# Kernel optimization log

Measured on AMD Instinct MI355X. Metric: run time of the kernel, lower is better.

## Reference

```python
import jax, jax.numpy as jnp
import numpy as np

B_GRAPHS = 256      # graphs per batch
NPG = 256           # nodes per graph
EXTENT = 32.0       # coordinate extent
K1 = 5              # kernel size per dim
KK = K1 * K1        # 25 weight matrices (dim=2)


def _cartesian(pos, row, col, ev):
    # pseudo-coords: relative cartesian, globally rescaled into [0,1]
    d = pos[col] - pos[row]                                   # [E,2]
    m = jnp.max(jnp.where(ev[:, None] > 0, jnp.abs(d), 0.0))
    return d / (2.0 * m + 1e-12) + 0.5


def _spline_conv(x, row, col, pseudo, ev, W, root, bias, n):
    # degree-1 open B-spline basis, 4 nonzero corners per edge (dim=2)
    v = pseudo * (K1 - 1)
    i0 = jnp.clip(jnp.floor(v), 0, K1 - 2).astype(jnp.int32)  # [E,2]
    f = v - i0
    xin = x[col]                                              # [E,Fin] gather
    acc = jnp.zeros((n * KK, x.shape[1]), x.dtype)
    for sx in (0, 1):
        for sy in (0, 1):
            idx = (i0[:, 0] + sx) * K1 + (i0[:, 1] + sy)      # flat kernel id
            wx = f[:, 0] if sx else 1.0 - f[:, 0]
            wy = f[:, 1] if sy else 1.0 - f[:, 1]
            b = wx * wy * ev
            acc = acc.at[row * KK + idx].add(b[:, None] * xin)
    acc = acc.reshape(n, KK, x.shape[1])                      # [n,25,Fin]
    deg = jax.ops.segment_sum(ev, row, num_segments=n)
    out = jnp.einsum('nki,kio->no', acc, W) / jnp.maximum(deg, 1.0)[:, None]
    return out + x @ root + bias


def _grid_pool(x, pos, row, col, ev, nv, size):
    g = int(EXTENT // size)
    c = jnp.clip(jnp.floor(pos / size).astype(jnp.int32), 0, g - 1)
    cluster = (jnp.arange(x.shape[0], dtype=jnp.int32) * 0)  # placeholder
    cell = c[:, 0] * g + c[:, 1]
    nb = x.shape[0] // 1  # nodes
    # batch id of each node = node's graph; recover from fixed layout
    # (cluster id = graph * g*g + cell)
    per_graph = nb // B_GRAPHS
    gb = jnp.arange(nb, dtype=jnp.int32) // per_graph
    cluster = gb * (g * g) + cell
    Nc = B_GRAPHS * g * g
    seg = jnp.where(nv > 0, cluster, Nc)                      # invalid -> dummy
    xm = jax.ops.segment_max(jnp.where(nv[:, None] > 0, x, -jnp.inf), seg,
                             num_segments=Nc + 1)[:Nc]
    cnt = jax.ops.segment_sum(nv, seg, num_segments=Nc + 1)[:Nc]
    nv2 = (cnt > 0).astype(x.dtype)
    x2 = jnp.where(nv2[:, None] > 0, xm, 0.0)
    pos2 = jax.ops.segment_sum(pos * nv[:, None], seg, num_segments=Nc + 1)[:Nc]
    pos2 = pos2 / jnp.maximum(cnt, 1.0)[:, None]
    batch2 = jnp.arange(Nc, dtype=jnp.int32) // (g * g)
    # remap + coalesce edges (drop self-loops and duplicates, fixed shapes)
    r2 = cluster[row]
    c2 = cluster[col]
    ev2 = (ev > 0) & (r2 != c2)
    key = jnp.where(ev2, r2 * Nc + c2, Nc * Nc)
    order = jnp.argsort(key)
    skey = key[order]
    dup = jnp.concatenate([jnp.zeros((1,), bool), skey[1:] == skey[:-1]])
    ev3 = ((skey < Nc * Nc) & ~dup).astype(x.dtype)
    return x2, pos2, r2[order], c2[order], ev3, batch2, nv2


def _forward(x, position, edge_index, batch, W1, root1, b1, W2, root2, b2,
             W3, root3, b3, fc_w, fc_b):
    row, col = edge_index[0], edge_index[1]
    E, N = row.shape[0], x.shape[0]
    ev = jnp.ones((E,), x.dtype)
    nv = jnp.ones((N,), x.dtype)
    ps = _cartesian(position, row, col, ev)
    h = jax.nn.elu(_spline_conv(x, row, col, ps, ev, W1, root1, b1, N))
    h, pos, row, col, ev, batch2, nv = _grid_pool(h, position, row, col, ev, nv, 4.0)
    ps = _cartesian(pos, row, col, ev)
    h = jax.nn.elu(_spline_conv(h, row, col, ps, ev, W2, root2, b2, h.shape[0]))
    h, pos, row, col, ev, batch2, nv = _grid_pool(h, pos, row, col, ev, nv, 8.0)
    ps = _cartesian(pos, row, col, ev)
    h = jax.nn.elu(_spline_conv(h, row, col, ps, ev, W3, root3, b3, h.shape[0]))
    # scatter_mean over graphs (only non-empty clusters count)
    gsum = jax.ops.segment_sum(h * nv[:, None], batch2, num_segments=B_GRAPHS)
    gcnt = jax.ops.segment_sum(nv, batch2, num_segments=B_GRAPHS)
    gfeat = gsum / jnp.maximum(gcnt, 1.0)[:, None]
    # dropout is identity in eval mode
    logits = gfeat @ fc_w + fc_b
    return jax.nn.log_softmax(logits, axis=1)


def setup_inputs() -> dict:
    DEG = 16
    N = B_GRAPHS * NPG
    E = N * DEG
    key = jax.random.key(0)
    ks = jax.random.split(key, 14)
    x = jax.random.uniform(ks[0], (N, 1), jnp.float32)
    position = jax.random.uniform(ks[1], (N, 2), jnp.float32) * EXTENT
    src = jax.random.randint(ks[2], (E,), 0, N, dtype=jnp.int32)
    tgt = (src // NPG) * NPG + jax.random.randint(ks[3], (E,), 0, NPG, dtype=jnp.int32)
    edge_index = jnp.stack([tgt, src])  # row = target, col = source
    batch = jnp.arange(N, dtype=jnp.int32) // NPG
    s = 0.1
    W1 = jax.random.normal(ks[4], (KK, 1, 32), jnp.float32) * s
    root1 = jax.random.normal(ks[5], (1, 32), jnp.float32) * s
    b1 = jnp.zeros((32,), jnp.float32)
    W2 = jax.random.normal(ks[6], (KK, 32, 64), jnp.float32) * s
    root2 = jax.random.normal(ks[7], (32, 64), jnp.float32) * s
    b2 = jnp.zeros((64,), jnp.float32)
    W3 = jax.random.normal(ks[8], (KK, 64, 128), jnp.float32) * s
    root3 = jax.random.normal(ks[9], (64, 128), jnp.float32) * s
    b3 = jnp.zeros((128,), jnp.float32)
    fc_w = jax.random.normal(ks[10], (128, 10), jnp.float32) * s
    fc_b = jnp.zeros((10,), jnp.float32)
    return dict(x=x, position=position, edge_index=edge_index, batch=batch,
                W1=W1, root1=root1, b1=b1, W2=W2, root2=root2, b2=b2,
                W3=W3, root3=root3, b3=b3, fc_w=fc_w, fc_b=fc_b)


def reference(x, position, edge_index, batch, W1, root1, b1, W2, root2, b2,
              W3, root3, b3, fc_w, fc_b):
    return _forward(x, position, edge_index, batch, W1, root1, b1,
                    W2, root2, b2, W3, root3, b3, fc_w, fc_b)
```

## Files before the change

### kernel.cpp

```cpp
#include <hip/hip_runtime.h>
#include <math.h>

constexpr int NN  = 65536;
constexpr int EE  = 1048576;
constexpr int NG  = 256;
constexpr int NC1 = 16384;
constexpr int NC2 = 4096;
constexpr int EPB = EE / 256;

constexpr size_t O_SCAL  = 0;
constexpr size_t O_GTOT  = 256;
constexpr size_t O_CNT2  = O_GTOT + 1024;
constexpr size_t O_PS2   = O_CNT2 + (size_t)NC2*4;
constexpr size_t Z_END   = O_PS2  + (size_t)NC2*8;
constexpr size_t O_XM2   = Z_END;
constexpr size_t O_GOFF  = O_XM2  + (size_t)NC2*64*4;
constexpr size_t O_BB    = O_GOFF + 1280;
constexpr size_t O_BE    = O_BB   + (size_t)256*256*4;
constexpr size_t O_XP1   = O_BE   + (size_t)EE*2;
constexpr size_t O_POS1  = O_XP1  + (size_t)NC1*32*4;
constexpr size_t O_NV1   = O_POS1 + (size_t)NC1*8;
constexpr size_t O_ADJ2  = O_NV1  + (size_t)NC1*4;
constexpr size_t O_OFF2S = O_ADJ2 + (size_t)NG*4096;
constexpr size_t O_DEG2I = O_OFF2S+ (size_t)NC1*4;
constexpr size_t O_CL2   = O_DEG2I+ (size_t)NC1*4;
constexpr size_t O_XP2   = O_CL2  + (size_t)NC1*4;
constexpr size_t O_POS2  = O_XP2  + (size_t)NC2*64*4;
constexpr size_t O_NV2   = O_POS2 + (size_t)NC2*8;
constexpr size_t O_ADJ3  = O_NV2  + (size_t)NC2*4;
constexpr size_t O_OFF3S = O_ADJ3 + (size_t)NG*256;
constexpr size_t O_DEG3I = O_OFF3S+ (size_t)NC2*4;
constexpr size_t O_H3    = O_DEG3I+ (size_t)NC2*4;
constexpr size_t O_W2Q   = O_H3   + (size_t)NC2*128*4;
constexpr size_t O_W3Q   = O_W2Q  + 102400;
constexpr size_t O_R2T   = O_W3Q  + 409600;
constexpr size_t O_R3T   = O_R2T  + 8192;

typedef __fp16   pk16x2 __attribute__((ext_vector_type(2)));
typedef _Float16 h16x2  __attribute__((ext_vector_type(2)));

__device__ __forceinline__ float eluf(float x){ return x > 0.f ? x : expm1f(x); }

__device__ __forceinline__ void atomic_max_pos(float* a, float v){
    atomicMax((unsigned int*)a, __float_as_uint(v));
}
__device__ __forceinline__ void atomic_max_f32(float* a, float v){
    unsigned int b = __float_as_uint(v);
    if (b & 0x80000000u) atomicMin((unsigned int*)a, b);
    else                 atomicMax((int*)a, (int)b);
}

__device__ __forceinline__ unsigned int pack2(float a, float b){
    pk16x2 h = __builtin_amdgcn_cvt_pkrtz(a, b);
    return __builtin_bit_cast(unsigned int, h);
}
__device__ __forceinline__ unsigned short f2h(float v){
    pk16x2 h = __builtin_amdgcn_cvt_pkrtz(v, v);
    return (unsigned short)(__builtin_bit_cast(unsigned int, h) & 0xFFFFu);
}
__device__ __forceinline__ float dot2u(unsigned int a, unsigned int b, float c){
#if __has_builtin(__builtin_amdgcn_fdot2)
    return __builtin_amdgcn_fdot2(__builtin_bit_cast(h16x2, a),
                                  __builtin_bit_cast(h16x2, b), c, false);
#else
    h16x2 ha = __builtin_bit_cast(h16x2, a), hb = __builtin_bit_cast(h16x2, b);
    return c + (float)ha[0]*(float)hb[0] + (float)ha[1]*(float)hb[1];
#endif
}

struct Crn { int ix, iy; float fx, fy; };
__device__ __forceinline__ Crn mk_corners(float dx, float dy, float m){
    float inv = 1.0f / (2.0f*m + 1e-12f);
    float vx = (dx*inv + 0.5f) * 4.0f;
    float vy = (dy*inv + 0.5f) * 4.0f;
    Crn c;
    c.ix = min(max((int)floorf(vx), 0), 3);
    c.iy = min(max((int)floorf(vy), 0), 3);
    c.fx = vx - (float)c.ix;
    c.fy = vy - (float)c.iy;
    return c;
}

#define BLOCK_MAX_AND_ATOMIC(val, dst)                                   \
    {   __shared__ float _s[256];                                        \
        _s[threadIdx.x] = (val); __syncthreads();                        \
        for (int _w = 128; _w > 0; _w >>= 1){                            \
            if (threadIdx.x < _w)                                        \
                _s[threadIdx.x] = fmaxf(_s[threadIdx.x], _s[threadIdx.x+_w]); \
            __syncthreads();                                             \
        }                                                                \
        if (threadIdx.x == 0) atomic_max_pos((dst), _s[0]); }

__global__ __launch_bounds__(256) void k_pass1(
        const int* __restrict__ ei, const float* __restrict__ pos,
        float* m1, int* gtot, int* bb,
        const float* __restrict__ W2, const float* __restrict__ W3,
        const float* __restrict__ root2, const float* __restrict__ root3,
        unsigned short* __restrict__ w2q, unsigned short* __restrict__ w3q,
        float* __restrict__ r2t, float* __restrict__ r3t){
    __shared__ int h[256];
    if (blockIdx.x >= 256){
        int idx = (blockIdx.x - 256)*256 + threadIdx.x;
        if (idx < 51200){
            int k = idx >> 6, o = idx & 63;
            w2q[(size_t)((k>>3)*64 + o)*8 + (k&7)] = f2h(W2[idx]);
        }
        int i3 = idx - 51200;
        if (i3 >= 0 && i3 < 204800){
            int k = i3 >> 7, o = i3 & 127;
            w3q[(size_t)((k>>3)*128 + o)*8 + (k&7)] = f2h(W3[i3]);
        }
        int ir2 = idx - 256000;
        if (ir2 >= 0 && ir2 < 2048){
            int i = ir2 >> 6, o = ir2 & 63;
            r2t[o*32 + i] = root2[ir2];
        }
        int ir3 = idx - 258048;
        if (ir3 >= 0 && ir3 < 8192){
            int i = ir3 >> 7, o = ir3 & 127;
            r3t[o*64 + i] = root3[ir3];
        }
        return;
    }
    h[threadIdx.x] = 0; __syncthreads();
    int base = blockIdx.x * EPB;
    float loc = 0.f;
    for (int i = threadIdx.x; i < EPB; i += 256){
        int e = base + i;
        int r = ei[e], c = ei[EE + e];
        float dx = pos[2*c]   - pos[2*r];
        float dy = pos[2*c+1] - pos[2*r+1];
        loc = fmaxf(loc, fmaxf(fabsf(dx), fabsf(dy)));
        atomicAdd(&h[r >> 8], 1);
    }
    __syncthreads();
    bb[blockIdx.x*256 + threadIdx.x] = atomicAdd(&gtot[threadIdx.x], h[threadIdx.x]);
    BLOCK_MAX_AND_ATOMIC(loc, m1);
}

__global__ void k_gscan(const int* __restrict__ gtot, int* goff){
    __shared__ int s[256];
    int t = threadIdx.x;
    int v0 = gtot[t];
    s[t] = v0; __syncthreads();
    for (int d = 1; d < 256; d <<= 1){
        int u = (t >= d) ? s[t-d] : 0;
        __syncthreads();
        s[t] += u;
        __syncthreads();
    }
    goff[t] = s[t] - v0;
    if (t == 255) goff[256] = s[t];
}

__global__ __launch_bounds__(256) void k_pass2(const int* __restrict__ ei,
                                               const int* __restrict__ goff,
                                               const int* __restrict__ bb,
                                               unsigned short* __restrict__ be){
    __shared__ int cur[256];
    cur[threadIdx.x] = 0; __syncthreads();
    int base = blockIdx.x * EPB;
    for (int i = threadIdx.x; i < EPB; i += 256){
        int e = base + i;
        int r = ei[e], c = ei[EE + e];
        int g = r >> 8;
        int l = atomicAdd(&cur[g], 1);
        be[goff[g] + bb[blockIdx.x*256 + g] + l] =
            (unsigned short)((r & 255) | ((c & 255) << 8));
    }
}

__global__ __launch_bounds__(1024) void k_graph1(
        const unsigned short* __restrict__ be, const int* __restrict__ goff,
        const float* __restrict__ pos, const float* __restrict__ x,
        const float* __restrict__ m1p, const float* __restrict__ W1,
        const float* __restrict__ root1, const float* __restrict__ b1,
        float* __restrict__ xp1, float* __restrict__ pos1g, float* __restrict__ nv1,
        unsigned char* __restrict__ adj2b, int* __restrict__ off2s,
        int* __restrict__ deg2i, float* m2p){
    __shared__ float acc[256*25];
    __shared__ float posx[256], posy[256], xL[256];
    __shared__ int   cl1L[256], degL[256];
    __shared__ float sW[800];
    __shared__ unsigned int bitL[128];
    __shared__ float xmL[64*32];
    __shared__ int   cntL[64];
    __shared__ float psx[64], psy[64];
    __shared__ float p1x[64], p1y[64];
    __shared__ int   rpre[64];
    __shared__ float mred[64];

    int t = threadIdx.x, g = blockIdx.x;
    if (t < 800) sW[t] = W1[t];
    for (int i = t; i < 6400; i += 1024) acc[i] = 0.f;
    if (t < 256){
        float px = pos[2*(g*256 + t)], py = pos[2*(g*256 + t) + 1];
        posx[t] = px; posy[t] = py;
        xL[t]   = x[g*256 + t];
        degL[t] = 0;
        int cx = min(max((int)floorf(px*0.25f), 0), 7);
        int cy = min(max((int)floorf(py*0.25f), 0), 7);
        cl1L[t] = cx*8 + cy;
    }
    if (t < 128) bitL[t] = 0u;
    if (t < 64){ cntL[t] = 0; psx[t] = 0.f; psy[t] = 0.f; }
    for (int i = t; i < 2048; i += 1024) xmL[i] = -INFINITY;
    __syncthreads();

    float mm = *m1p;
    int e1 = goff[g+1];
    for (int p = goff[g] + t; p < e1; p += 1024){
        unsigned int b = be[p];
        int rl = b & 255, cl = (b >> 8) & 255;
        float dx = posx[cl] - posx[rl], dy = posy[cl] - posy[rl];
        Crn cr = mk_corners(dx, dy, mm);
        float xin = xL[cl];
        int ab = rl*25 + cr.ix*5 + cr.iy;
        atomicAdd(&acc[ab],   (1.f-cr.fx)*(1.f-cr.fy)*xin);
        atomicAdd(&acc[ab+1], (1.f-cr.fx)*cr.fy*xin);
        atomicAdd(&acc[ab+5], cr.fx*(1.f-cr.fy)*xin);
        atomicAdd(&acc[ab+6], cr.fx*cr.fy*xin);
        atomicAdd(&degL[rl], 1);
        int r2 = cl1L[rl], c2 = cl1L[cl];
        if (r2 != c2){
            int bit = r2*64 + c2;
            atomicOr(&bitL[bit >> 5], 1u << (bit & 31));
        }
    }
    __syncthreads();

    {
        int n = t >> 2, q = t & 3;
        float accR[25];
        #pragma unroll
        for (int k = 0; k < 25; k++) accR[k] = acc[n*25 + k];
        float inv = 1.f / fmaxf((float)degL[n], 1.f);
        float xr  = xL[n];
        int   cl  = cl1L[n];
        if (q == 0){
            atomicAdd(&cntL[cl], 1);
            atomicAdd(&psx[cl], posx[n]);
            atomicAdd(&psy[cl], posy[n]);
        }
        #pragma unroll
        for (int oo = 0; oo < 8; oo++){
            int o = q*8 + oo;
            float s = 0.f;
            #pragma unroll
            for (int k = 0; k < 25; k++) s += accR[k]*sW[k*32 + o];
            float out = eluf(s*inv + xr*root1[o] + b1[o]);
            atomic_max_f32(&xmL[cl*32 + o], out);
        }
    }
    __syncthreads();

    if (t < 64){
        float cnt = (float)cntL[t];
        float inv = 1.f / fmaxf(cnt, 1.f);
        p1x[t] = psx[t]*inv; p1y[t] = psy[t]*inv;
        pos1g[2*(g*64 + t)]     = p1x[t];
        pos1g[2*(g*64 + t) + 1] = p1y[t];
        nv1[g*64 + t] = (cnt > 0.f) ? 1.f : 0.f;
    }
    __syncthreads();
    for (int i = t; i < 2048; i += 1024){
        int c = i >> 5;
        xp1[g*2048 + i] = (cntL[c] > 0) ? xmL[i] : 0.f;
    }

    if (t < 64) rpre[t] = __popc(bitL[2*t]) + __popc(bitL[2*t+1]);
    __syncthreads();
    for (int d = 1; d < 64; d <<= 1){
        int v = 0;
        if (t < 64 && t >= d) v = rpre[t-d];
        __syncthreads();
        if (t < 64) rpre[t] += v;
        __syncthreads();
    }
    float m2loc = 0.f;
    if (t < 64){
        unsigned int w0 = bitL[2*t], w1 = bitL[2*t+1];
        int dg = __popc(w0) + __popc(w1);
        int baseo = rpre[t] - dg;
        off2s[g*64 + t] = g*4096 + baseo;
        deg2i[g*64 + t] = dg;
        int j = g*4096 + baseo;
        float rx = p1x[t], ry = p1y[t];
        while (w0){
            int b = __ffs(w0) - 1; w0 &= w0 - 1;
            adj2b[j++] = (unsigned char)b;
            m2loc = fmaxf(m2loc, fmaxf(fabsf(p1x[b]-rx), fabsf(p1y[b]-ry)));
        }
        while (w1){
            int b = __ffs(w1) - 1; w1 &= w1 - 1;
            int c = 32 + b;
            adj2b[j++] = (unsigned char)c;
            m2loc = fmaxf(m2loc, fmaxf(fabsf(p1x[c]-rx), fabsf(p1y[c]-ry)));
        }
        mred[t] = m2loc;
    }
    __syncthreads();
    if (t == 0){
        float v = mred[0];
        for (int i = 1; i < 64; i++) v = fmaxf(v, mred[i]);
        atomic_max_pos(m2p, v);
    }
}

__global__ __launch_bounds__(512) void k_conv2(
        const int* __restrict__ off2s, const int* __restrict__ deg2i,
        const unsigned char* __restrict__ adj2b, const float* __restrict__ pos1g,
        const float* __restrict__ m2p, const float* __restrict__ xp1,
        const unsigned short* __restrict__ w2q, const float* __restrict__ r2t,
        const float* __restrict__ b2, const float* __restrict__ nv1,
        int* __restrict__ cl2, float* cnt2, float* ps2, float* xm2){
    __shared__ __align__(16) unsigned int amu[16*400];
    __shared__ __align__(16) float xpL[64*32];
    __shared__ float p1x[64], p1y[64];
    int t = threadIdx.x;
    int g = blockIdx.x >> 2, sub = blockIdx.x & 3;
    for (int i = t; i < 2048; i += 512) xpL[i] = xp1[g*2048 + i];
    if (t < 64){ p1x[t] = pos1g[2*(g*64+t)]; p1y[t] = pos1g[2*(g*64+t)+1]; }
    __syncthreads();
    int grp = t >> 5, lane = t & 31;
    {
        int rl = sub*16 + grp;
        int r  = g*64 + rl;
        int s0 = off2s[r], n = deg2i[r];
        float rx = p1x[rl], ry = p1y[rl];
        float mm = *m2p;
        float inv = 1.0f / (2.0f*mm + 1e-12f);
        float acc[25];
        #pragma unroll
        for (int k = 0; k < 25; k++) acc[k] = 0.f;
        for (int j = 0; j < n; ++j){
            int cLoc = adj2b[s0 + j];
            float vx = ((p1x[cLoc] - rx)*inv + 0.5f)*4.0f;
            float vy = ((p1y[cLoc] - ry)*inv + 0.5f)*4.0f;
            float xin = xpL[cLoc*32 + lane];
            float wxx[5], wy[5];
            #pragma unroll
            for (int k = 0; k < 5; k++){
                wxx[k] = fmaxf(0.f, 1.f - fabsf(vx - (float)k)) * xin;
                wy[k]  = fmaxf(0.f, 1.f - fabsf(vy - (float)k));
            }
            #pragma unroll
            for (int kx = 0; kx < 5; kx++)
                #pragma unroll
                for (int ky = 0; ky < 5; ky++)
                    acc[kx*5+ky] = fmaf(wxx[kx], wy[ky], acc[kx*5+ky]);
        }
        unsigned int* dst = &amu[grp*400];
        #pragma unroll
        for (int k = 0; k < 25; k++){
            float other = __shfl_xor(acc[k], 1, 64);
            if (!(lane & 1)) dst[k*16 + (lane >> 1)] = pack2(acc[k], other);
        }
    }
    __syncthreads();
    int o = t & 63, mg = t >> 6;
    const unsigned int* a0 = amu + mg*400;
    const unsigned int* a1 = amu + (mg+8)*400;
    const uint4* wq = (const uint4*)w2q;
    float sA0=0.f, sA1=0.f, sB0=0.f, sB1=0.f;
    for (int kp8 = 0; kp8 < 100; kp8++){
        uint4 wv = wq[kp8*64 + o];
        uint4 av = *(const uint4*)(a0 + kp8*4);
        uint4 bv = *(const uint4*)(a1 + kp8*4);
        sA0 = dot2u(av.x, wv.x, sA0); sA1 = dot2u(av.y, wv.y, sA1);
        sA0 = dot2u(av.z, wv.z, sA0); sA1 = dot2u(av.w, wv.w, sA1);
        sB0 = dot2u(bv.x, wv.x, sB0); sB1 = dot2u(bv.y, wv.y, sB1);
        sB0 = dot2u(bv.z, wv.z, sB0); sB1 = dot2u(bv.w, wv.w, sB1);
    }
    float sAB[2] = {sA0 + sA1, sB0 + sB1};
    #pragma unroll
    for (int h = 0; h < 2; ++h){
        int rl = sub*16 + mg + h*8;
        int rr = g*64 + rl;
        float s  = sAB[h];
        float dg = fmaxf((float)deg2i[rr], 1.f);
        float rt = 0.f;
        #pragma unroll
        for (int i = 0; i < 32; i += 4){
            float4 rv = *(const float4*)&r2t[o*32 + i];
            float4 xv = *(const float4*)&xpL[rl*32 + i];
            rt += rv.x*xv.x + rv.y*xv.y + rv.z*xv.z + rv.w*xv.w;
        }
        float val = eluf(s/dg + rt + b2[o]);
        float px = p1x[rl], py = p1y[rl];
        int cx = min(max((int)floorf(px*0.125f), 0), 3);
        int cy = min(max((int)floorf(py*0.125f), 0), 3);
        int cl = g*16 + cx*4 + cy;
        if (o == 0) cl2[rr] = cl;
        if (nv1[rr] > 0.f){
            if (o == 0){
                atomicAdd(&cnt2[cl], 1.f);
                atomicAdd(&ps2[2*cl],   px);
                atomicAdd(&ps2[2*cl+1], py);
            }
            atomic_max_f32(&xm2[cl*64 + o], val);
        }
    }
}

__global__ __launch_bounds__(256) void k_lvl3(
        const int* __restrict__ off2s, const int* __restrict__ deg2i,
        const unsigned char* __restrict__ adj2b, const int* __restrict__ cl2,
        const float* __restrict__ cnt2, const float* __restrict__ ps2,
        const float* __restrict__ xm2,
        float* __restrict__ xp2, float* __restrict__ pos2g, float* __restrict__ nv2,
        unsigned char* __restrict__ adj3b, int* __restrict__ off3s,
        int* __restrict__ deg3i, float* m3p){
    __shared__ int cl2L[64];
    __shared__ unsigned int bit3[8];
    __shared__ float p2x[16], p2y[16];
    __shared__ int rpre[16];
    int t = threadIdx.x, g = blockIdx.x;
    if (t < 64) cl2L[t] = cl2[g*64 + t] & 15;
    if (t < 8)  bit3[t] = 0u;
    if (t < 16){
        float cnt = cnt2[g*16 + t];
        float inv = 1.f / fmaxf(cnt, 1.f);
        p2x[t] = ps2[2*(g*16+t)]*inv;
        p2y[t] = ps2[2*(g*16+t)+1]*inv;
        pos2g[2*(g*16+t)]   = p2x[t];
        pos2g[2*(g*16+t)+1] = p2y[t];
        nv2[g*16 + t] = (cnt > 0.f) ? 1.f : 0.f;
    }
    for (int i = t; i < 1024; i += 256){
        int c = i >> 6;
        xp2[g*1024 + i] = (cnt2[g*16 + c] > 0.f) ? xm2[g*1024 + i] : 0.f;
    }
    __syncthreads();
    if (t < 64){
        int s0 = off2s[g*64 + t], n = deg2i[g*64 + t];
        int r3 = cl2L[t];
        for (int j = 0; j < n; ++j){
            int c3 = cl2L[adj2b[s0 + j]];
            if (r3 != c3){
                int bit = r3*16 + c3;
                atomicOr(&bit3[bit >> 5], 1u << (bit & 31));
            }
        }
    }
    __syncthreads();
    if (t < 16)
        rpre[t] = __popc((bit3[t >> 1] >> ((t & 1)*16)) & 0xFFFFu);
    __syncthreads();
    for (int d = 1; d < 16; d <<= 1){
        int v = 0;
        if (t < 16 && t >= d) v = rpre[t-d];
        __syncthreads();
        if (t < 16) rpre[t] += v;
        __syncthreads();
    }
    float m3loc = 0.f;
    if (t < 16){
        unsigned int w = (bit3[t >> 1] >> ((t & 1)*16)) & 0xFFFFu;
        int dg = __popc(w);
        int baseo = rpre[t] - dg;
        off3s[g*16 + t] = g*256 + baseo;
        deg3i[g*16 + t] = dg;
        int j = g*256 + baseo;
        float rx = p2x[t], ry = p2y[t];
        while (w){
            int b = __ffs(w) - 1; w &= w - 1;
            adj3b[j++] = (unsigned char)b;
            m3loc = fmaxf(m3loc, fmaxf(fabsf(p2x[b]-rx), fabsf(p2y[b]-ry)));
        }
    }
    BLOCK_MAX_AND_ATOMIC(m3loc, m3p);
}

__global__ __launch_bounds__(512) void k_conv3(
        const int* __restrict__ off3s, const int* __restrict__ deg3i,
        const unsigned char* __restrict__ adj3b, const float* __restrict__ pos2g,
        const float* __restrict__ m3p, const float* __restrict__ xp2,
        const unsigned short* __restrict__ w3q, const float* __restrict__ r3t,
        const float* __restrict__ b3, float* __restrict__ h3){
    __shared__ __align__(16) unsigned int amu[8*800];
    __shared__ __align__(16) float xpL[16*64];
    __shared__ float p2x[16], p2y[16];
    int t = threadIdx.x;
    int g = blockIdx.x >> 1, sub = blockIdx.x & 1;
    for (int i = t; i < 1024; i += 512) xpL[i] = xp2[g*1024 + i];
    if (t < 16){ p2x[t] = pos2g[2*(g*16+t)]; p2y[t] = pos2g[2*(g*16+t)+1]; }
    __syncthreads();
    int grp = t >> 6, lane = t & 63;
    {
        int rl = sub*8 + grp;
        int r  = g*16 + rl;
        int s0 = off3s[r], n = deg3i[r];
        float rx = p2x[rl], ry = p2y[rl];
        float mm = *m3p;
        float inv = 1.0f / (2.0f*mm + 1e-12f);
        float acc[25];
        #pragma unroll
        for (int k = 0; k < 25; k++) acc[k] = 0.f;
        for (int j = 0; j < n; ++j){
            int cLoc = adj3b[s0 + j];
            float vx = ((p2x[cLoc] - rx)*inv + 0.5f)*4.0f;
            float vy = ((p2y[cLoc] - ry)*inv + 0.5f)*4.0f;
            float xin = xpL[cLoc*64 + lane];
            float wxx[5], wy[5];
            #pragma unroll
            for (int k = 0; k < 5; k++){
                wxx[k] = fmaxf(0.f, 1.f - fabsf(vx - (float)k)) * xin;
                wy[k]  = fmaxf(0.f, 1.f - fabsf(vy - (float)k));
            }
            #pragma unroll
            for (int kx = 0; kx < 5; kx++)
                #pragma unroll
                for (int ky = 0; ky < 5; ky++)
                    acc[kx*5+ky] = fmaf(wxx[kx], wy[ky], acc[kx*5+ky]);
        }
        unsigned int* dst = &amu[grp*800];
        #pragma unroll
        for (int k = 0; k < 25; k++){
            float other = __shfl_xor(acc[k], 1, 64);
            if (!(lane & 1)) dst[k*32 + (lane >> 1)] = pack2(acc[k], other);
        }
    }
    __syncthreads();
    int o = t & 127, mg = t >> 7;
    const unsigned int* a0 = amu + mg*800;
    const unsigned int* a1 = amu + (mg+4)*800;
    const uint4* wq = (const uint4*)w3q;
    float sA0=0.f, sA1=0.f, sB0=0.f, sB1=0.f;
    for (int kp8 = 0; kp8 < 200; kp8++){
        uint4 wv = wq[kp8*128 + o];
        uint4 av = *(const uint4*)(a0 + kp8*4);
        uint4 bv = *(const uint4*)(a1 + kp8*4);
        sA0 = dot2u(av.x, wv.x, sA0); sA1 = dot2u(av.y, wv.y, sA1);
        sA0 = dot2u(av.z, wv.z, sA0); sA1 = dot2u(av.w, wv.w, sA1);
        sB0 = dot2u(bv.x, wv.x, sB0); sB1 = dot2u(bv.y, wv.y, sB1);
        sB0 = dot2u(bv.z, wv.z, sB0); sB1 = dot2u(bv.w, wv.w, sB1);
    }
    float sAB[2] = {sA0 + sA1, sB0 + sB1};
    #pragma unroll
    for (int h = 0; h < 2; ++h){
        int rl = sub*8 + mg + h*4;
        int rr = g*16 + rl;
        float s  = sAB[h];
        float dg = fmaxf((float)deg3i[rr], 1.f);
        float rt = 0.f;
        #pragma unroll
        for (int i = 0; i < 64; i += 4){
            float4 rv = *(const float4*)&r3t[o*64 + i];
            float4 xv = *(const float4*)&xpL[rl*64 + i];
            rt += rv.x*xv.x + rv.y*xv.y + rv.z*xv.z + rv.w*xv.w;
        }
        h3[rr*128 + o] = eluf(s/dg + rt + b3[o]);
    }
}

__global__ void k_readout(const float* __restrict__ h3, const float* __restrict__ nv2,
                          const float* __restrict__ fcw, const float* __restrict__ fcb,
                          float* out){
    int g = blockIdx.x, t = threadIdx.x;
    __shared__ float gf[128];
    __shared__ float lg[10];
    __shared__ float lse;
    float s = 0.f, cnt = 0.f;
    for (int j = 0; j < 16; j++){
        int c = g*16 + j;
        float nv = nv2[c];
        s += h3[c*128 + t] * nv;
        cnt += nv;
    }
    gf[t] = s / fmaxf(cnt, 1.f);
    __syncthreads();
    if (t < 10){
        float l = fcb[t];
        for (int f = 0; f < 128; f++) l += gf[f]*fcw[f*10 + t];
        lg[t] = l;
    }
    __syncthreads();
    if (t == 0){
        float mx = -INFINITY;
        for (int o = 0; o < 10; o++) mx = fmaxf(mx, lg[o]);
        float ss = 0.f;
        for (int o = 0; o < 10; o++) ss += expf(lg[o] - mx);
        lse = mx + logf(ss);
    }
    __syncthreads();
    if (t < 10) out[g*10 + t] = lg[t] - lse;
}

extern "C" void kernel_launch(void* const* d_in, const int* in_sizes, int n_in,
                              void* d_out, int out_size, void* d_ws, size_t ws_size,
                              hipStream_t stream){
    const float* x     = (const float*)d_in[0];
    const float* posi  = (const float*)d_in[1];
    const int*   ei    = (const int*)  d_in[2];
    const float* W1    = (const float*)d_in[4];
    const float* root1 = (const float*)d_in[5];
    const float* b1    = (const float*)d_in[6];
    const float* W2    = (const float*)d_in[7];
    const float* root2 = (const float*)d_in[8];
    const float* b2    = (const float*)d_in[9];
    const float* W3    = (const float*)d_in[10];
    const float* root3 = (const float*)d_in[11];
    const float* b3    = (const float*)d_in[12];
    const float* fcw   = (const float*)d_in[13];
    const float* fcb   = (const float*)d_in[14];
    float* out = (float*)d_out;

    char* ws = (char*)d_ws;
    float*          m1    = (float*)(ws + O_SCAL);
    float*          m2    = m1 + 1;
    float*          m3    = m1 + 2;
    int*            gtot  = (int*)  (ws + O_GTOT);
    float*          cnt2  = (float*)(ws + O_CNT2);
    float*          ps2   = (float*)(ws + O_PS2);
    float*          xm2   = (float*)(ws + O_XM2);
    int*            goff  = (int*)  (ws + O_GOFF);
    int*            bb    = (int*)  (ws + O_BB);
    unsigned short* be    = (unsigned short*)(ws + O_BE);
    float*          xp1   = (float*)(ws + O_XP1);
    float*          pos1g = (float*)(ws + O_POS1);
    float*          nv1   = (float*)(ws + O_NV1);
    unsigned char*  adj2b = (unsigned char*)(ws + O_ADJ2);
    int*            off2s = (int*)  (ws + O_OFF2S);
    int*            deg2i = (int*)  (ws + O_DEG2I);
    int*            cl2   = (int*)  (ws + O_CL2);
    float*          xp2   = (float*)(ws + O_XP2);
    float*          pos2g = (float*)(ws + O_POS2);
    float*          nv2   = (float*)(ws + O_NV2);
    unsigned char*  adj3b = (unsigned char*)(ws + O_ADJ3);
    int*            off3s = (int*)  (ws + O_OFF3S);
    int*            deg3i = (int*)  (ws + O_DEG3I);
    float*          h3    = (float*)(ws + O_H3);
    unsigned short* w2q   = (unsigned short*)(ws + O_W2Q);
    unsigned short* w3q   = (unsigned short*)(ws + O_W3Q);
    float*          r2t   = (float*)(ws + O_R2T);
    float*          r3t   = (float*)(ws + O_R3T);

    hipMemsetAsync(ws, 0, Z_END, stream);
    hipMemsetAsync(xm2, 0xFF, (size_t)NC2*64*4, stream);

    k_pass1<<<256 + 1040, 256, 0, stream>>>(ei, posi, m1, gtot, bb,
                                            W2, W3, root2, root3, w2q, w3q, r2t, r3t);
    k_gscan<<<1, 256, 0, stream>>>(gtot, goff);
    k_pass2<<<256, 256, 0, stream>>>(ei, goff, bb, be);

    k_graph1<<<NG, 1024, 0, stream>>>(be, goff, posi, x, m1, W1, root1, b1,
                                      xp1, pos1g, nv1, adj2b, off2s, deg2i, m2);

    k_conv2<<<NC1/16, 512, 0, stream>>>(off2s, deg2i, adj2b, pos1g, m2, xp1,
                                        w2q, r2t, b2, nv1, cl2, cnt2, ps2, xm2);

    k_lvl3<<<NG, 256, 0, stream>>>(off2s, deg2i, adj2b, cl2, cnt2, ps2, xm2,
                                   xp2, pos2g, nv2, adj3b, off3s, deg3i, m3);

    k_conv3<<<NC2/8, 512, 0, stream>>>(off3s, deg3i, adj3b, pos2g, m3, xp2,
                                       w3q, r3t, b3, h3);

    k_readout<<<256, 128, 0, stream>>>(h3, nv2, fcw, fcb, out);
}
```

Before: 290.2 us.

## Use MFMA f16 matrix cores for conv2/conv3 weight and root GEMMs

Replaces the fdot2-based per-thread dot products in conv2 and conv3 with 16x16x32 f16 MFMA instructions. The weights and root matrices are pre-packed into the MFMA operand layout, and the root term is folded in as extra K-steps. Degree normalisation now happens before the f16 packing. Edge basis weights are computed once per lane and broadcast with shuffles rather than recomputed per edge. conv3 now handles a whole graph per block. This cuts ALU work on the dense stages, at the cost of rounding the root inputs to f16 and changing the launch shape.

Result: faster. 274.6 us (-5.4%).

```diff
diff --git a/kernel.cpp b/kernel.cpp
--- a/kernel.cpp
+++ b/kernel.cpp
@@ -33,11 +33,12 @@
 constexpr size_t O_H3    = O_DEG3I+ (size_t)NC2*4;
 constexpr size_t O_W2Q   = O_H3   + (size_t)NC2*128*4;
 constexpr size_t O_W3Q   = O_W2Q  + 102400;
-constexpr size_t O_R2T   = O_W3Q  + 409600;
-constexpr size_t O_R3T   = O_R2T  + 8192;
+constexpr size_t O_RT2   = O_W3Q  + 409600;
+constexpr size_t O_RT3   = O_RT2  + 4096;
 
 typedef __fp16   pk16x2 __attribute__((ext_vector_type(2)));
-typedef _Float16 h16x2  __attribute__((ext_vector_type(2)));
+typedef _Float16 f16x8  __attribute__((ext_vector_type(8)));
+typedef float    f32x4  __attribute__((ext_vector_type(4)));
 
 __device__ __forceinline__ float eluf(float x){ return x > 0.f ? x : expm1f(x); }
 
@@ -54,18 +55,9 @@
     pk16x2 h = __builtin_amdgcn_cvt_pkrtz(a, b);
     return __builtin_bit_cast(unsigned int, h);
 }
-__device__ __forceinline__ unsigned short f2h(float v){
-    pk16x2 h = __builtin_amdgcn_cvt_pkrtz(v, v);
-    return (unsigned short)(__builtin_bit_cast(unsigned int, h) & 0xFFFFu);
-}
-__device__ __forceinline__ float dot2u(unsigned int a, unsigned int b, float c){
-#if __has_builtin(__builtin_amdgcn_fdot2)
-    return __builtin_amdgcn_fdot2(__builtin_bit_cast(h16x2, a),
-                                  __builtin_bit_cast(h16x2, b), c, false);
-#else
-    h16x2 ha = __builtin_bit_cast(h16x2, a), hb = __builtin_bit_cast(h16x2, b);
-    return c + (float)ha[0]*(float)hb[0] + (float)ha[1]*(float)hb[1];
-#endif
+__device__ __forceinline__ f32x4 mfma16(uint4 a, uint4 b, f32x4 c){
+    return __builtin_amdgcn_mfma_f32_16x16x32_f16(
+        __builtin_bit_cast(f16x8, a), __builtin_bit_cast(f16x8, b), c, 0, 0, 0);
 }
 
 struct Crn { int ix, iy; float fx, fy; };
@@ -96,29 +88,36 @@
         float* m1, int* gtot, int* bb,
         const float* __restrict__ W2, const float* __restrict__ W3,
         const float* __restrict__ root2, const float* __restrict__ root3,
-        unsigned short* __restrict__ w2q, unsigned short* __restrict__ w3q,
-        float* __restrict__ r2t, float* __restrict__ r3t){
+        unsigned int* __restrict__ w2q, unsigned int* __restrict__ w3q,
+        unsigned int* __restrict__ rt2q, unsigned int* __restrict__ rt3q){
     __shared__ int h[256];
     if (blockIdx.x >= 256){
         int idx = (blockIdx.x - 256)*256 + threadIdx.x;
-        if (idx < 51200){
-            int k = idx >> 6, o = idx & 63;
-            w2q[(size_t)((k>>3)*64 + o)*8 + (k&7)] = f2h(W2[idx]);
-        }
-        int i3 = idx - 51200;
-        if (i3 >= 0 && i3 < 204800){
-            int k = i3 >> 7, o = i3 & 127;
-            w3q[(size_t)((k>>3)*128 + o)*8 + (k&7)] = f2h(W3[i3]);
-        }
-        int ir2 = idx - 256000;
-        if (ir2 >= 0 && ir2 < 2048){
-            int i = ir2 >> 6, o = ir2 & 63;
-            r2t[o*32 + i] = root2[ir2];
-        }
-        int ir3 = idx - 258048;
-        if (ir3 >= 0 && ir3 < 8192){
-            int i = ir3 >> 7, o = ir3 & 127;
-            r3t[o*64 + i] = root3[ir3];
+        if (idx < 25600){
+            int tt = idx/6400, r = idx%6400, i = r/256, r2 = r%256;
+            int l = r2>>2, j = r2&3;
+            int o = tt*16 + (l&15);
+            int Kb = i*32 + (l>>4)*8 + 2*j;
+            w2q[idx] = pack2(W2[Kb*64 + o], W2[(Kb+1)*64 + o]);
+        } else if (idx < 128000){
+            int d = idx - 25600;
+            int tt = d/12800, r = d%12800, kc = r/256, r2 = r%256;
+            int l = r2>>2, j = r2&3;
+            int o = tt*16 + (l&15);
+            int Kb = kc*32 + (l>>4)*8 + 2*j;
+            w3q[d] = pack2(W3[Kb*128 + o], W3[(Kb+1)*128 + o]);
+        } else if (idx < 129024){
+            int d = idx - 128000;
+            int tt = d/256, r2 = d%256, l = r2>>2, j = r2&3;
+            int o = tt*16 + (l&15);
+            int k = (l>>4)*8 + 2*j;
+            rt2q[d] = pack2(root2[k*64 + o], root2[(k+1)*64 + o]);
+        } else if (idx < 133120){
+            int d = idx - 129024;
+            int tt = d/512, kc = (d/256)&1, r2 = d%256, l = r2>>2, j = r2&3;
+            int o = tt*16 + (l&15);
+            int k = kc*32 + (l>>4)*8 + 2*j;
+            rt3q[d] = pack2(root3[k*128 + o], root3[(k+1)*128 + o]);
         }
         return;
     }
@@ -311,94 +310,122 @@
         const int* __restrict__ off2s, const int* __restrict__ deg2i,
         const unsigned char* __restrict__ adj2b, const float* __restrict__ pos1g,
         const float* __restrict__ m2p, const float* __restrict__ xp1,
-        const unsigned short* __restrict__ w2q, const float* __restrict__ r2t,
+        const unsigned int* __restrict__ wq2, const unsigned int* __restrict__ rt2q,
         const float* __restrict__ b2, const float* __restrict__ nv1,
         int* __restrict__ cl2, float* cnt2, float* ps2, float* xm2){
-    __shared__ __align__(16) unsigned int amu[16*400];
-    __shared__ __align__(16) float xpL[64*32];
+    __shared__ unsigned int amu[16*404];
+    __shared__ float xpL[64*32];
+    __shared__ unsigned int xq[16*20];
+    __shared__ float pc[8*256];
     __shared__ float p1x[64], p1y[64];
     int t = threadIdx.x;
     int g = blockIdx.x >> 2, sub = blockIdx.x & 3;
     for (int i = t; i < 2048; i += 512) xpL[i] = xp1[g*2048 + i];
     if (t < 64){ p1x[t] = pos1g[2*(g*64+t)]; p1y[t] = pos1g[2*(g*64+t)+1]; }
     __syncthreads();
+    if (t < 256){
+        int m = t >> 4, jj = t & 15;
+        int c = sub*16 + m;
+        xq[m*20 + jj] = pack2(xpL[c*32 + 2*jj], xpL[c*32 + 2*jj + 1]);
+    }
     int grp = t >> 5, lane = t & 31;
     {
         int rl = sub*16 + grp;
         int r  = g*64 + rl;
-        int s0 = off2s[r], n = deg2i[r];
+        int s0 = off2s[r], nd = deg2i[r];
         float rx = p1x[rl], ry = p1y[rl];
-        float mm = *m2p;
-        float inv = 1.0f / (2.0f*mm + 1e-12f);
+        float invm = 1.0f / (2.0f*(*m2p) + 1e-12f);
         float acc[25];
         #pragma unroll
         for (int k = 0; k < 25; k++) acc[k] = 0.f;
-        for (int j = 0; j < n; ++j){
-            int cLoc = adj2b[s0 + j];
-            float vx = ((p1x[cLoc] - rx)*inv + 0.5f)*4.0f;
-            float vy = ((p1y[cLoc] - ry)*inv + 0.5f)*4.0f;
-            float xin = xpL[cLoc*32 + lane];
-            float wxx[5], wy[5];
+        for (int base = 0; base < nd; base += 32){
+            int e = base + lane;
+            int myc = 0;
+            float wxl[5], wyl[5];
             #pragma unroll
-            for (int k = 0; k < 5; k++){
-                wxx[k] = fmaxf(0.f, 1.f - fabsf(vx - (float)k)) * xin;
-                wy[k]  = fmaxf(0.f, 1.f - fabsf(vy - (float)k));
+            for (int k = 0; k < 5; k++){ wxl[k] = 0.f; wyl[k] = 0.f; }
+            if (e < nd){
+                myc = adj2b[s0 + e];
+                float vx = ((p1x[myc]-rx)*invm + 0.5f)*4.0f;
+                float vy = ((p1y[myc]-ry)*invm + 0.5f)*4.0f;
+                #pragma unroll
+                for (int k = 0; k < 5; k++){
+                    wxl[k] = fmaxf(0.f, 1.f - fabsf(vx - (float)k));
+                    wyl[k] = fmaxf(0.f, 1.f - fabsf(vy - (float)k));
+                }
             }
-            #pragma unroll
-            for (int kx = 0; kx < 5; kx++)
+            int cnt = min(32, nd - base);
+            for (int j = 0; j < cnt; ++j){
+                int c = __shfl(myc, j, 32);
+                float xin = xpL[c*32 + lane];
+                float xv[5], yv[5];
                 #pragma unroll
-                for (int ky = 0; ky < 5; ky++)
-                    acc[kx*5+ky] = fmaf(wxx[kx], wy[ky], acc[kx*5+ky]);
-        }
-        unsigned int* dst = &amu[grp*400];
+                for (int k = 0; k < 5; k++){
+                    xv[k] = __shfl(wxl[k], j, 32) * xin;
+                    yv[k] = __shfl(wyl[k], j, 32);
+                }
+                #pragma unroll
+                for (int kx = 0; kx < 5; kx++)
+                    #pragma unroll
+                    for (int ky = 0; ky < 5; ky++)
+                        acc[kx*5+ky] = fmaf(xv[kx], yv[ky], acc[kx*5+ky]);
+            }
+        }
+        float invd = 1.f / fmaxf((float)nd, 1.f);
+        unsigned int* dst = &amu[grp*404];
         #pragma unroll
         for (int k = 0; k < 25; k++){
-            float other = __shfl_xor(acc[k], 1, 64);
-            if (!(lane & 1)) dst[k*16 + (lane >> 1)] = pack2(acc[k], other);
-        }
-    }
-    __syncthreads();
-    int o = t & 63, mg = t >> 6;
-    const unsigned int* a0 = amu + mg*400;
-    const unsigned int* a1 = amu + (mg+8)*400;
-    const uint4* wq = (const uint4*)w2q;
-    float sA0=0.f, sA1=0.f, sB0=0.f, sB1=0.f;
-    for (int kp8 = 0; kp8 < 100; kp8++){
-        uint4 wv = wq[kp8*64 + o];
-        uint4 av = *(const uint4*)(a0 + kp8*4);
-        uint4 bv = *(const uint4*)(a1 + kp8*4);
-        sA0 = dot2u(av.x, wv.x, sA0); sA1 = dot2u(av.y, wv.y, sA1);
-        sA0 = dot2u(av.z, wv.z, sA0); sA1 = dot2u(av.w, wv.w, sA1);
-        sB0 = dot2u(bv.x, wv.x, sB0); sB1 = dot2u(bv.y, wv.y, sB1);
-        sB0 = dot2u(bv.z, wv.z, sB0); sB1 = dot2u(bv.w, wv.w, sB1);
-    }
-    float sAB[2] = {sA0 + sA1, sB0 + sB1};
-    #pragma unroll
-    for (int h = 0; h < 2; ++h){
-        int rl = sub*16 + mg + h*8;
-        int rr = g*64 + rl;
-        float s  = sAB[h];
-        float dg = fmaxf((float)deg2i[rr], 1.f);
-        float rt = 0.f;
-        #pragma unroll
-        for (int i = 0; i < 32; i += 4){
-            float4 rv = *(const float4*)&r2t[o*32 + i];
-            float4 xv = *(const float4*)&xpL[rl*32 + i];
-            rt += rv.x*xv.x + rv.y*xv.y + rv.z*xv.z + rv.w*xv.w;
-        }
-        float val = eluf(s/dg + rt + b2[o]);
-        float px = p1x[rl], py = p1y[rl];
-        int cx = min(max((int)floorf(px*0.125f), 0), 3);
-        int cy = min(max((int)floorf(py*0.125f), 0), 3);
-        int cl = g*16 + cx*4 + cy;
-        if (o == 0) cl2[rr] = cl;
-        if (nv1[rr] > 0.f){
+            float a = acc[k]*invd;
+            float o2 = __shfl_xor(a, 1, 64);
+            if (!(lane & 1)) dst[k*16 + (lane >> 1)] = pack2(a, o2);
+        }
+    }
+    __syncthreads();
+    {
+        int w = t >> 6, l = t & 63;
+        int tt = w & 3, kh = w >> 2;
+        int m = l & 15, kb = l >> 4;
+        f32x4 cacc = {0.f, 0.f, 0.f, 0.f};
+        int ks0 = kh ? 12 : 0, ks1 = kh ? 25 : 12;
+        for (int i = ks0; i < ks1; ++i){
+            uint4 au = *(const uint4*)&amu[m*404 + i*16 + kb*4];
+            uint4 bu = *(const uint4*)&wq2[((tt*25 + i)*64 + l)*4];
+            cacc = mfma16(au, bu, cacc);
+        }
+        if (kh == 0){
+            uint4 au = *(const uint4*)&xq[m*20 + kb*4];
+            uint4 bu = *(const uint4*)&rt2q[(tt*64 + l)*4];
+            cacc = mfma16(au, bu, cacc);
+        }
+        *(f32x4*)&pc[w*256 + l*4] = cacc;
+    }
+    __syncthreads();
+    {
+        int tt = t >> 7, q = t & 127;
+        int l = q & 63, rh = q >> 6;
+        #pragma unroll
+        for (int u = 0; u < 2; ++u){
+            int r_ = rh*2 + u;
+            int m = (l >> 4)*4 + r_;
+            int o = tt*16 + (l & 15);
+            float val = pc[tt*256 + l*4 + r_] + pc[(tt+4)*256 + l*4 + r_];
+            val = eluf(val + b2[o]);
+            int rl = sub*16 + m;
+            int rr = g*64 + rl;
+            float px = p1x[rl], py = p1y[rl];
+            int cx = min(max((int)floorf(px*0.125f), 0), 3);
+            int cy = min(max((int)floorf(py*0.125f), 0), 3);
+            int cl = g*16 + cx*4 + cy;
+            float nv = nv1[rr];
             if (o == 0){
-                atomicAdd(&cnt2[cl], 1.f);
-                atomicAdd(&ps2[2*cl],   px);
-                atomicAdd(&ps2[2*cl+1], py);
+                cl2[rr] = cl;
+                if (nv > 0.f){
+                    atomicAdd(&cnt2[cl], 1.f);
+                    atomicAdd(&ps2[2*cl],   px);
+                    atomicAdd(&ps2[2*cl+1], py);
+                }
             }
-            atomic_max_f32(&xm2[cl*64 + o], val);
+            if (nv > 0.f) atomic_max_f32(&xm2[cl*64 + o], val);
         }
     }
 }
@@ -476,81 +503,95 @@
         const int* __restrict__ off3s, const int* __restrict__ deg3i,
         const unsigned char* __restrict__ adj3b, const float* __restrict__ pos2g,
         const float* __restrict__ m3p, const float* __restrict__ xp2,
-        const unsigned short* __restrict__ w3q, const float* __restrict__ r3t,
+        const unsigned int* __restrict__ wq3, const unsigned int* __restrict__ rt3q,
         const float* __restrict__ b3, float* __restrict__ h3){
-    __shared__ __align__(16) unsigned int amu[8*800];
-    __shared__ __align__(16) float xpL[16*64];
+    __shared__ unsigned int amu[16*804];
+    __shared__ float xpL[16*64];
+    __shared__ unsigned int xq[16*36];
     __shared__ float p2x[16], p2y[16];
-    int t = threadIdx.x;
-    int g = blockIdx.x >> 1, sub = blockIdx.x & 1;
+    int t = threadIdx.x, g = blockIdx.x;
     for (int i = t; i < 1024; i += 512) xpL[i] = xp2[g*1024 + i];
     if (t < 16){ p2x[t] = pos2g[2*(g*16+t)]; p2y[t] = pos2g[2*(g*16+t)+1]; }
     __syncthreads();
+    {
+        int m = t >> 5, jj = t & 31;
+        xq[m*36 + jj] = pack2(xpL[m*64 + 2*jj], xpL[m*64 + 2*jj + 1]);
+    }
     int grp = t >> 6, lane = t & 63;
+    float invm = 1.0f / (2.0f*(*m3p) + 1e-12f);
+    for (int cc = 0; cc < 2; ++cc){
+        int rl = grp + cc*8;
+        int r  = g*16 + rl;
+        int s0 = off3s[r], nd = deg3i[r];
+        float rx = p2x[rl], ry = p2y[rl];
+        float acc[25];
+        #pragma unroll
+        for (int k = 0; k < 25; k++) acc[k] = 0.f;
+        for (int base = 0; base < nd; base += 64){
+            int e = base + lane;
+            int myc = 0;
+            float wxl[5], wyl[5];
+            #pragma unroll
+            for (int k = 0; k < 5; k++){ wxl[k] = 0.f; wyl[k] = 0.f; }
+            if (e < nd){
+                myc = adj3b[s0 + e];
+                float vx = ((p2x[myc]-rx)*invm + 0.5f)*4.0f;
+                float vy = ((p2y[myc]-ry)*invm + 0.5f)*4.0f;
+                #pragma unroll
+                for (int k = 0; k < 5; k++){
+                    wxl[k] = fmaxf(0.f, 1.f - fabsf(vx - (float)k));
+                    wyl[k] = fmaxf(0.f, 1.f - fabsf(vy - (float)k));
+                }
+            }
+            int cnt = min(64, nd - base);
+            for (int j = 0; j < cnt; ++j){
+                int c = __shfl(myc, j, 64);
+                float xin = xpL[c*64 + lane];
+                float xv[5], yv[5];
+                #pragma unroll
+                for (int k = 0; k < 5; k++){
+                    xv[k] = __shfl(wxl[k], j, 64) * xin;
+                    yv[k] = __shfl(wyl[k], j, 64);
+                }
+                #pragma unroll
+                for (int kx = 0; kx < 5; kx++)
+                    #pragma unroll
+                    for (int ky = 0; ky < 5; ky++)
+                        acc[kx*5+ky] = fmaf(xv[kx], yv[ky], acc[kx*5+ky]);
+            }
+        }
+        float invd = 1.f / fmaxf((float)nd, 1.f);
+        unsigned int* dst = &amu[rl*804];
+        #pragma unroll
+        for (int k = 0; k < 25; k++){
+            float a = acc[k]*invd;
+            float o2 = __shfl_xor(a, 1, 64);
+            if (!(lane & 1)) dst[k*32 + (lane >> 1)] = pack2(a, o2);
+        }
+    }
+    __syncthreads();
     {
-        int rl = sub*8 + grp;
-        int r  = g*16 + rl;
-        int s0 = off3s[r], n = deg3i[r];
-        float rx = p2x[rl], ry = p2y[rl];
-        float mm = *m3p;
-        float inv = 1.0f / (2.0f*mm + 1e-12f);
-        float acc[25];
-        #pragma unroll
-        for (int k = 0; k < 25; k++) acc[k] = 0.f;
-        for (int j = 0; j < n; ++j){
-            int cLoc = adj3b[s0 + j];
-            float vx = ((p2x[cLoc] - rx)*inv + 0.5f)*4.0f;
-            float vy = ((p2y[cLoc] - ry)*inv + 0.5f)*4.0f;
-            float xin = xpL[cLoc*64 + lane];
-            float wxx[5], wy[5];
-            #pragma unroll
-            for (int k = 0; k < 5; k++){
-                wxx[k] = fmaxf(0.f, 1.f - fabsf(vx - (float)k)) * xin;
-                wy[k]  = fmaxf(0.f, 1.f - fabsf(vy - (float)k));
-            }
-            #pragma unroll
-            for (int kx = 0; kx < 5; kx++)
-                #pragma unroll
-                for (int ky = 0; ky < 5; ky++)
-                    acc[kx*5+ky] = fmaf(wxx[kx], wy[ky], acc[kx*5+ky]);
-        }
-        unsigned int* dst = &amu[grp*800];
-        #pragma unroll
-        for (int k = 0; k < 25; k++){
-            float other = __shfl_xor(acc[k], 1, 64);
-            if (!(lane & 1)) dst[k*32 + (lane >> 1)] = pack2(acc[k], other);
-        }
-    }
-    __syncthreads();
-    int o = t & 127, mg = t >> 7;
-    const unsigned int* a0 = amu + mg*800;
-    const unsigned int* a1 = amu + (mg+4)*800;
-    const uint4* wq = (const uint4*)w3q;
-    float sA0=0.f, sA1=0.f, sB0=0.f, sB1=0.f;
-    for (int kp8 = 0; kp8 < 200; kp8++){
-        uint4 wv = wq[kp8*128 + o];
-        uint4 av = *(const uint4*)(a0 + kp8*4);
-        uint4 bv = *(const uint4*)(a1 + kp8*4);
-        sA0 = dot2u(av.x, wv.x, sA0); sA1 = dot2u(av.y, wv.y, sA1);
-        sA0 = dot2u(av.z, wv.z, sA0); sA1 = dot2u(av.w, wv.w, sA1);
-        sB0 = dot2u(bv.x, wv.x, sB0); sB1 = dot2u(bv.y, wv.y, sB1);
-        sB0 = dot2u(bv.z, wv.z, sB0); sB1 = dot2u(bv.w, wv.w, sB1);
-    }
-    float sAB[2] = {sA0 + sA1, sB0 + sB1};
-    #pragma unroll
-    for (int h = 0; h < 2; ++h){
-        int rl = sub*8 + mg + h*4;
-        int rr = g*16 + rl;
-        float s  = sAB[h];
-        float dg = fmaxf((float)deg3i[rr], 1.f);
-        float rt = 0.f;
-        #pragma unroll
-        for (int i = 0; i < 64; i += 4){
-            float4 rv = *(const float4*)&r3t[o*64 + i];
-            float4 xv = *(const float4*)&xpL[rl*64 + i];
-            rt += rv.x*xv.x + rv.y*xv.y + rv.z*xv.z + rv.w*xv.w;
-        }
-        h3[rr*128 + o] = eluf(s/dg + rt + b3[o]);
+        int w = t >> 6, l = t & 63;
+        int m = l & 15, kb = l >> 4;
+        f32x4 cacc = {0.f, 0.f, 0.f, 0.f};
+        for (int kc = 0; kc < 50; ++kc){
+            uint4 au = *(const uint4*)&amu[m*804 + kc*16 + kb*4];
+            uint4 bu = *(const uint4*)&wq3[((w*50 + kc)*64 + l)*4];
+            cacc = mfma16(au, bu, cacc);
+        }
+        #pragma unroll
+        for (int kc = 0; kc < 2; ++kc){
+            uint4 au = *(const uint4*)&xq[m*36 + kc*16 + kb*4];
+            uint4 bu = *(const uint4*)&rt3q[((w*2 + kc)*64 + l)*4];
+            cacc = mfma16(au, bu, cacc);
+        }
+        int o = w*16 + (l & 15);
+        float bb3 = b3[o];
+        #pragma unroll
+        for (int r_ = 0; r_ < 4; ++r_){
+            int m2_ = (l >> 4)*4 + r_;
+            h3[(g*16 + m2_)*128 + o] = eluf(cacc[r_] + bb3);
+        }
     }
 }
 
@@ -631,16 +672,16 @@
     int*            off3s = (int*)  (ws + O_OFF3S);
     int*            deg3i = (int*)  (ws + O_DEG3I);
     float*          h3    = (float*)(ws + O_H3);
-    unsigned short* w2q   = (unsigned short*)(ws + O_W2Q);
-    unsigned short* w3q   = (unsigned short*)(ws + O_W3Q);
-    float*          r2t   = (float*)(ws + O_R2T);
-    float*          r3t   = (float*)(ws + O_R3T);
+    unsigned int*   w2q   = (unsigned int*)(ws + O_W2Q);
+    unsigned int*   w3q   = (unsigned int*)(ws + O_W3Q);
+    unsigned int*   rt2q  = (unsigned int*)(ws + O_RT2);
+    unsigned int*   rt3q  = (unsigned int*)(ws + O_RT3);
 
     hipMemsetAsync(ws, 0, Z_END, stream);
     hipMemsetAsync(xm2, 0xFF, (size_t)NC2*64*4, stream);
 
-    k_pass1<<<256 + 1040, 256, 0, stream>>>(ei, posi, m1, gtot, bb,
-                                            W2, W3, root2, root3, w2q, w3q, r2t, r3t);
+    k_pass1<<<256 + 520, 256, 0, stream>>>(ei, posi, m1, gtot, bb,
+                                           W2, W3, root2, root3, w2q, w3q, rt2q, rt3q);
     k_gscan<<<1, 256, 0, stream>>>(gtot, goff);
     k_pass2<<<256, 256, 0, stream>>>(ei, goff, bb, be);
 
@@ -648,13 +689,13 @@
                                       xp1, pos1g, nv1, adj2b, off2s, deg2i, m2);
 
     k_conv2<<<NC1/16, 512, 0, stream>>>(off2s, deg2i, adj2b, pos1g, m2, xp1,
-                                        w2q, r2t, b2, nv1, cl2, cnt2, ps2, xm2);
+                                        w2q, rt2q, b2, nv1, cl2, cnt2, ps2, xm2);
 
     k_lvl3<<<NG, 256, 0, stream>>>(off2s, deg2i, adj2b, cl2, cnt2, ps2, xm2,
                                    xp2, pos2g, nv2, adj3b, off3s, deg3i, m3);
 
-    k_conv3<<<NC2/8, 512, 0, stream>>>(off3s, deg3i, adj3b, pos2g, m3, xp2,
-                                       w3q, r3t, b3, h3);
+    k_conv3<<<NG, 512, 0, stream>>>(off3s, deg3i, adj3b, pos2g, m3, xp2,
+                                    w3q, rt3q, b3, h3);
 
     k_readout<<<256, 128, 0, stream>>>(h3, nv2, fcw, fcb, out);
 }
```
